# Kernel optimization log

Hardware: AMD Instinct MI355X
Metric: run time of the kernel (lower is better)

Reference implementation:

```python
import jax, jax.numpy as jnp
import numpy as np
import math

B, M, DM = 4, 4096, 1024
H, HD = 16, 64            # head_dim = hidden_dim // num_heads
SEG, DIL = 128, 2         # segment_size, dilation_rate
BLOCK_M = 64              # kernel query-block size (min(64, M))
SCALE = HD ** -0.5


def _hilbert_map(seq_len):
    # Faithful port of create_hilbert_mapping_fixed (boustrophedon scan).
    if seq_len <= 64:
        return np.arange(seq_len, dtype=np.int32)
    g = int(math.ceil(math.sqrt(seq_len)))
    mp = np.zeros(seq_len, dtype=np.int64)
    idx = 0
    for row in range(g):
        cols = range(g) if row % 2 == 0 else range(g - 1, -1, -1)
        for col in cols:
            if idx < seq_len:
                lp = row * g + col
                if lp < seq_len:
                    mp[lp] = idx
                    idx += 1
    for i in range(seq_len):
        if i >= idx:
            mp[i] = i
    return mp.astype(np.int32)


def setup_inputs() -> dict:
    key = jax.random.key(0)
    k1, k2, k3 = jax.random.split(key, 3)
    x = jax.random.normal(k1, (B, M, DM), jnp.float32)
    Wqkv = jax.random.normal(k2, (3 * DM, DM), jnp.float32) * 0.02
    Wout = jax.random.normal(k3, (DM, DM), jnp.float32) * 0.02
    hmap = jnp.asarray(_hilbert_map(M))
    return {"x": x, "Wqkv": Wqkv, "Wout": Wout, "hmap": hmap}


def _hilbert_attention(x, Wqkv, Wout, hmap):
    Bn, Mn, _ = x.shape
    qkv = x @ Wqkv.T                                   # [B,M,3*DM]
    qkv = qkv.reshape(Bn, Mn, 3, H, HD).transpose(2, 0, 3, 1, 4)
    q, k, v = qkv[0], qkv[1], qkv[2]                   # [B,H,M,HD]

    S = Mn // SEG           # number of segments
    T = SEG // DIL          # keys per segment (dilated offsets 0, DIL, 2*DIL, ...)
    NB = SEG // BLOCK_M     # query blocks per segment

    # Queries gathered through Hilbert map, pre-scaled (as in kernel).
    qh = q[:, :, hmap, :] * SCALE                      # [B,H,M,HD]

    # Dilated key positions per segment, gathered through Hilbert map.
    key_pos = (jnp.arange(S)[:, None] * SEG + jnp.arange(T)[None, :] * DIL).reshape(-1)
    kh = k[:, :, hmap[key_pos], :].reshape(Bn, H, S, T, HD)
    vh = v[:, :, hmap[key_pos], :].reshape(Bn, H, S, T, HD)

    # Scores per (query-block within segment, key): [B,H,S,NB,BLOCK_M,T]
    qs = qh.reshape(Bn, H, S, NB, BLOCK_M, HD)
    scores = jnp.einsum('bhsnqd,bhstd->bhsnqt', qs, kh)

    # Kernel quirk (faithful): per-KEY max taken over the 64-query block,
    # exp accumulated without rescaling -> NOT a true softmax.
    c = jnp.max(scores, axis=4, keepdims=True)         # max over query block
    w = jnp.exp(scores - c)
    num = jnp.einsum('bhsnqt,bhstd->bhsnqd', w, vh)
    den = 1e-10 + jnp.sum(w, axis=-1, keepdims=True)
    out = (num / den).reshape(Bn, H, Mn, HD)

    # Stored at linear (non-Hilbert) positions, then merged heads + out proj.
    out = out.transpose(0, 2, 1, 3).reshape(Bn, Mn, H * HD)
    return out @ Wout.T


def reference(x, Wqkv, Wout, hmap):
    return _hilbert_attention(x, Wqkv, Wout, hmap)
```

## Files before the change

kernel.cpp:

```cpp
#include <hip/hip_runtime.h>
#include <hip/hip_bf16.h>

#define BB 4
#define MM 4096
#define DM 1024
#define NH 16
#define HDIM 64
#define SEGSZ 128
#define NSEG 32
#define ROWS (BB*MM)
#define QKVC (3*DM)
#define KVROWS (BB*MM/2)
#define KVLD 2048
#define NX4  (ROWS*DM/4)
#define NW14 (QKVC*DM/4)
#define NW24 (DM*DM/4)

typedef __attribute__((ext_vector_type(8))) short bf16x8;
typedef __attribute__((ext_vector_type(4))) float f32x4;

__device__ inline unsigned short f2bf(float f) {
  __hip_bfloat16 h = __float2bfloat16(f);
  return *reinterpret_cast<unsigned short*>(&h);
}

__device__ __forceinline__ void gld16(const ushort* g, ushort* l) {
  __builtin_amdgcn_global_load_lds(
      (const __attribute__((address_space(1))) unsigned int*)g,
      (__attribute__((address_space(3))) unsigned int*)l,
      16, 0, 0);
}

__global__ __launch_bounds__(256) void cvt_all(const float4* __restrict__ x,
                                               const float4* __restrict__ w1,
                                               const float4* __restrict__ w2,
                                               ushort4* __restrict__ xo,
                                               ushort4* __restrict__ w1o,
                                               ushort4* __restrict__ w2o) {
  int i = blockIdx.x * 256 + threadIdx.x;
  const float4* src; ushort4* dst; int off;
  if (i < NX4)              { src = x;  dst = xo;  off = i; }
  else if (i < NX4 + NW14)  { src = w1; dst = w1o; off = i - NX4; }
  else                      { src = w2; dst = w2o; off = i - NX4 - NW14; }
  float4 v = src[off];
  ushort4 o;
  o.x = f2bf(v.x); o.y = f2bf(v.y); o.z = f2bf(v.z); o.w = f2bf(v.w);
  dst[off] = o;
}

__global__ __launch_bounds__(512) void gemm_qkv(const ushort* __restrict__ xbf,
                                                const ushort* __restrict__ wqkv,
                                                ushort* __restrict__ qhb,
                                                ushort* __restrict__ kvb,
                                                const int* __restrict__ hmap) {
  __shared__ __align__(16) ushort sAB[65536];
  __shared__ int sRow[256];

  const int blk = blockIdx.x;
  const int tid = threadIdx.x;
  const int lane = tid & 63;
  const int wave = tid >> 6;
  const int m16 = lane & 15;
  const int quad = lane >> 4;
  const int wm = wave >> 2;
  const int wn = wave & 3;

  const ushort* Bmat; ushort* C; int row0, col0, N;
  if (blk < 256) {
    row0 = (blk >> 2) * 256; col0 = (blk & 3) * 256;
    Bmat = wqkv; C = qhb; N = DM;
  } else {
    int j = blk - 256;
    row0 = (j >> 3) * 256; col0 = (j & 7) * 256;
    Bmat = wqkv + (size_t)DM * DM; C = kvb; N = KVLD;
  }

  if (tid < 256) {
    int m = row0 + tid, xrow;
    if (blk < 256) {
      int b = m >> 12, p = m & 4095;
      xrow = (b << 12) + hmap[p];
    } else {
      int b = m >> 11, idx = m & 2047;
      int ss = idx >> 6, tt = idx & 63;
      xrow = (b << 12) + hmap[ss * SEGSZ + 2 * tt];
    }
    sRow[tid] = xrow;
  }
  __syncthreads();

  const int f0 = wave * 64 + lane, f1 = 512 + f0;
  const int r0 = f0 >> 2, c0 = (f0 & 3) ^ ((f0 >> 3) & 3);
  const int r1 = f1 >> 2, c1 = (f1 & 3) ^ ((f1 >> 3) & 3);
  const ushort* pA0 = xbf + (size_t)sRow[r0] * DM + c0 * 8;
  const ushort* pA1 = xbf + (size_t)sRow[r1] * DM + c1 * 8;
  const ushort* pB0 = Bmat + (size_t)(col0 + r0) * DM + c0 * 8;
  const ushort* pB1 = Bmat + (size_t)(col0 + r1) * DM + c1 * 8;

  f32x4 acc[8][4] = {};

#define STAGE_A(T, KH, DB) do {                                              \
    gld16(pA0 + (T) * 64 + (KH) * 32,                                        \
          sAB + ((DB) * 2 + (KH)) * 8192 + wave * 512);                      \
    gld16(pA1 + (T) * 64 + (KH) * 32,                                        \
          sAB + ((DB) * 2 + (KH)) * 8192 + 4096 + wave * 512);               \
  } while (0)
#define STAGE_B(T, KH, DB) do {                                              \
    gld16(pB0 + (T) * 64 + (KH) * 32,                                        \
          sAB + 32768 + ((DB) * 2 + (KH)) * 8192 + wave * 512);              \
    gld16(pB1 + (T) * 64 + (KH) * 32,                                        \
          sAB + 32768 + ((DB) * 2 + (KH)) * 8192 + 4096 + wave * 512);       \
  } while (0)
#define VM6 asm volatile("s_waitcnt vmcnt(6)" ::: "memory")
#define VM8 asm volatile("s_waitcnt vmcnt(8)" ::: "memory")
#define VM0 asm volatile("s_waitcnt vmcnt(0)" ::: "memory")
#define NOPS ((void)0)

#define PH(TB, KH, CH, STAGE, VMA) do {                                      \
    const ushort* Ab = sAB + ((TB) * 2 + (KH)) * 8192;                       \
    const ushort* Bb = sAB + 32768 + ((TB) * 2 + (KH)) * 8192;               \
    bf16x8 af[8], bfv[2];                                                    \
    _Pragma("unroll")                                                        \
    for (int mf = 0; mf < 8; ++mf) {                                         \
      int r = wm * 128 + mf * 16 + m16;                                      \
      af[mf] = *(const bf16x8*)(Ab + r * 32 + ((quad ^ ((r >> 1) & 3)) << 3)); \
    }                                                                        \
    _Pragma("unroll")                                                        \
    for (int nf = 0; nf < 2; ++nf) {                                         \
      int r = wn * 64 + (CH) * 32 + nf * 16 + m16;                           \
      bfv[nf] = *(const bf16x8*)(Bb + r * 32 + ((quad ^ ((r >> 1) & 3)) << 3)); \
    }                                                                        \
    STAGE;                                                                   \
    VMA;                                                                     \
    __builtin_amdgcn_s_barrier();                                            \
    asm volatile("s_waitcnt lgkmcnt(0)" ::: "memory");                       \
    __builtin_amdgcn_sched_barrier(0);                                       \
    __builtin_amdgcn_s_setprio(1);                                           \
    _Pragma("unroll")                                                        \
    for (int mf = 0; mf < 8; ++mf)                                           \
      _Pragma("unroll")                                                      \
      for (int nf = 0; nf < 2; ++nf)                                         \
        acc[mf][(CH) * 2 + nf] = __builtin_amdgcn_mfma_f32_16x16x32_bf16(    \
            af[mf], bfv[nf], acc[mf][(CH) * 2 + nf], 0, 0, 0);               \
    __builtin_amdgcn_s_setprio(0);                                           \
    __builtin_amdgcn_s_barrier();                                            \
  } while (0)

  STAGE_A(0, 0, 0); STAGE_B(0, 0, 0);
  STAGE_A(0, 1, 0); STAGE_B(0, 1, 0);
  STAGE_A(1, 0, 1); STAGE_B(1, 0, 1);
  VM8;
  __builtin_amdgcn_s_barrier();

#pragma unroll 1
  for (int i = 0; i < 7; ++i) {
    const int t1 = 2 * i + 1, t2 = 2 * i + 2, t3 = 2 * i + 3;
    PH(0, 0, 0, STAGE_A(t1, 1, 1), NOPS);
    PH(0, 0, 1, STAGE_B(t1, 1, 1), VM6);
    PH(0, 1, 0, STAGE_A(t2, 0, 0), NOPS);
    PH(0, 1, 1, STAGE_B(t2, 0, 0), VM6);
    PH(1, 0, 0, STAGE_A(t2, 1, 0), NOPS);
    PH(1, 0, 1, STAGE_B(t2, 1, 0), VM6);
    PH(1, 1, 0, STAGE_A(t3, 0, 1), NOPS);
    PH(1, 1, 1, STAGE_B(t3, 0, 1), VM6);
  }
  PH(0, 0, 0, STAGE_A(15, 1, 1), NOPS);
  PH(0, 0, 1, STAGE_B(15, 1, 1), VM0);
  PH(0, 1, 0, NOPS, NOPS);
  PH(0, 1, 1, NOPS, NOPS);
  PH(1, 0, 0, NOPS, NOPS);
  PH(1, 0, 1, NOPS, NOPS);
  PH(1, 1, 0, NOPS, NOPS);
  PH(1, 1, 1, NOPS, NOPS);

#undef PH
#undef STAGE_A
#undef STAGE_B
#undef VM6
#undef VM8
#undef VM0
#undef NOPS

#pragma unroll
  for (int mf = 0; mf < 8; ++mf)
#pragma unroll
    for (int rr = 0; rr < 4; ++rr) {
      int row = row0 + wm * 128 + mf * 16 + quad * 4 + rr;
#pragma unroll
      for (int nf = 0; nf < 4; ++nf)
        C[(size_t)row * N + col0 + wn * 64 + nf * 16 + m16] = f2bf(acc[mf][nf][rr]);
    }
}

__global__ __launch_bounds__(256) void gemm_out(const ushort* __restrict__ A,
                                                const ushort* __restrict__ Bmat,
                                                float* __restrict__ C) {
  __shared__ __align__(16) ushort sA[128 * 32];
  __shared__ __align__(16) ushort sB[64 * 32];
  const int blk = blockIdx.x;
  const int row0 = (blk >> 4) * 128;
  const int col0 = (blk & 15) * 64;
  const int tid = threadIdx.x;
  const int lane = tid & 63;
  const int wave = tid >> 6;
  const int m16 = lane & 15;
  const int quad = lane >> 4;
  const int wr = (wave >> 1) * 64;
  const int wc = (wave & 1) * 32;

  f32x4 acc[4][2] = {};

  const int ch0 = wave * 64 + lane;
  const int ch1 = 256 + wave * 64 + lane;
  const int ra0 = ch0 >> 2, ka0 = (ch0 & 3) * 8;
  const int ra1 = ch1 >> 2, ka1 = (ch1 & 3) * 8;

  const ushort* pa0 = A + (size_t)(row0 + ra0) * DM + ka0;
  const ushort* pa1 = A + (size_t)(row0 + ra1) * DM + ka1;
  const ushort* pb0 = Bmat + (size_t)(col0 + ra0) * DM + ka0;
  ushort* lA0 = sA + wave * 512;
  ushort* lA1 = sA + 2048 + wave * 512;
  ushort* lB0 = sB + wave * 512;

  for (int kt = 0; kt < DM; kt += 32) {
    __syncthreads();
    gld16(pa0 + kt, lA0);
    gld16(pa1 + kt, lA1);
    gld16(pb0 + kt, lB0);
    __syncthreads();

    bf16x8 af[4], bfr[2];
#pragma unroll
    for (int i = 0; i < 4; ++i)
      af[i] = *(const bf16x8*)(sA + (wr + i * 16 + m16) * 32 + quad * 8);
#pragma unroll
    for (int j = 0; j < 2; ++j)
      bfr[j] = *(const bf16x8*)(sB + (wc + j * 16 + m16) * 32 + quad * 8);
#pragma unroll
    for (int i = 0; i < 4; ++i)
#pragma unroll
      for (int j = 0; j < 2; ++j)
        acc[i][j] = __builtin_amdgcn_mfma_f32_16x16x32_bf16(af[i], bfr[j], acc[i][j], 0, 0, 0);
  }

#pragma unroll
  for (int i = 0; i < 4; ++i)
#pragma unroll
    for (int r = 0; r < 4; ++r) {
      int row = row0 + wr + i * 16 + quad * 4 + r;
#pragma unroll
      for (int j = 0; j < 2; ++j)
        C[(size_t)row * DM + col0 + wc + j * 16 + m16] = acc[i][j][r];
    }
}

__global__ __launch_bounds__(256) void attn_kernel(const ushort* __restrict__ qh,
                                                   const ushort* __restrict__ kv,
                                                   ushort* __restrict__ out) {
  __shared__ __align__(16) ushort sQW[128 * 72];
  __shared__ __align__(16) ushort sK[64 * 72];
  __shared__ __align__(16) ushort sVT[64 * 72];
  __shared__ float sCmaxW[4 * 64];
  __shared__ float sDen[128];

  const int bid = blockIdx.x;
  const int s  = bid & 31;
  const int h  = (bid >> 5) & 15;
  const int b  = bid >> 9;
  const int tid = threadIdx.x;
  const int lane = tid & 63;
  const int wave = tid >> 6;
  const int m16 = lane & 15;
  const int quad = lane >> 4;
  const int qb = wave * 32;
  const int hb = wave >> 1;

  {
    const int qr = tid >> 1;
    const int qc = (tid & 1) * 32;
    const ushort* qrow = qh + (size_t)(b * MM + s * SEGSZ + qr) * DM + h * HDIM + qc;
    *(uint4*)(sQW + qr * 72 + qc)      = ((const uint4*)qrow)[0];
    *(uint4*)(sQW + qr * 72 + qc + 8)  = ((const uint4*)qrow)[1];
    *(uint4*)(sQW + qr * 72 + qc + 16) = ((const uint4*)qrow)[2];
    *(uint4*)(sQW + qr * 72 + qc + 24) = ((const uint4*)qrow)[3];

    const int r = tid >> 2;
    const int c = (tid & 3) * 16;
    const ushort* krow = kv + (size_t)(b * (MM/2) + s * 64 + r) * KVLD + h * HDIM + c;
    const ushort* vrow = krow + DM;
    *(uint4*)(sK + r * 72 + c)     = ((const uint4*)krow)[0];
    *(uint4*)(sK + r * 72 + c + 8) = ((const uint4*)krow)[1];
    ushort vv[16];
    *(uint4*)(vv)     = ((const uint4*)vrow)[0];
    *(uint4*)(vv + 8) = ((const uint4*)vrow)[1];
#pragma unroll
    for (int u = 0; u < 16; ++u) sVT[(c + u) * 72 + r] = vv[u];
  }
  __syncthreads();

  f32x4 sc[2][4];
  {
    bf16x8 aq[2][2], bk[4][2];
#pragma unroll
    for (int ks = 0; ks < 2; ++ks) {
#pragma unroll
      for (int ib = 0; ib < 2; ++ib)
        aq[ib][ks] = *(const bf16x8*)(sQW + (qb + ib * 16 + m16) * 72 + ks * 32 + quad * 8);
#pragma unroll
      for (int j = 0; j < 4; ++j)
        bk[j][ks] = *(const bf16x8*)(sK + (j * 16 + m16) * 72 + ks * 32 + quad * 8);
    }
#pragma unroll
    for (int ib = 0; ib < 2; ++ib)
#pragma unroll
      for (int j = 0; j < 4; ++j) {
        f32x4 a = {};
        a = __builtin_amdgcn_mfma_f32_16x16x32_bf16(aq[ib][0], bk[j][0], a, 0, 0, 0);
        a = __builtin_amdgcn_mfma_f32_16x16x32_bf16(aq[ib][1], bk[j][1], a, 0, 0, 0);
        sc[ib][j] = a * 0.125f;
      }
  }

#pragma unroll
  for (int j = 0; j < 4; ++j) {
    float m = -1e30f;
#pragma unroll
    for (int ib = 0; ib < 2; ++ib)
#pragma unroll
      for (int r = 0; r < 4; ++r) m = fmaxf(m, sc[ib][j][r]);
    m = fmaxf(m, __shfl_xor(m, 16));
    m = fmaxf(m, __shfl_xor(m, 32));
    if (quad == 0) sCmaxW[wave * 64 + j * 16 + m16] = m;
  }
  __syncthreads();

  {
    float part[2][4] = {};
#pragma unroll
    for (int j = 0; j < 4; ++j) {
      const int col = j * 16 + m16;
      float c0 = fmaxf(sCmaxW[hb * 128 + col], sCmaxW[hb * 128 + 64 + col]);
#pragma unroll
      for (int ib = 0; ib < 2; ++ib)
#pragma unroll
        for (int r = 0; r < 4; ++r) {
          float ww = __expf(sc[ib][j][r] - c0);
          sc[ib][j][r] = ww;
          part[ib][r] += ww;
        }
    }
#pragma unroll
    for (int ib = 0; ib < 2; ++ib)
#pragma unroll
      for (int r = 0; r < 4; ++r) {
        float p = part[ib][r];
        p += __shfl_xor(p, 1); p += __shfl_xor(p, 2);
        p += __shfl_xor(p, 4); p += __shfl_xor(p, 8);
        if (m16 == 0) sDen[qb + ib * 16 + quad * 4 + r] = p;
      }
#pragma unroll
    for (int ib = 0; ib < 2; ++ib)
#pragma unroll
      for (int j = 0; j < 4; ++j)
#pragma unroll
        for (int r = 0; r < 4; ++r)
          sQW[(qb + ib * 16 + quad * 4 + r) * 72 + j * 16 + m16] = f2bf(sc[ib][j][r]);
  }
  __syncthreads();

  f32x4 o[2][4] = {};
  {
    bf16x8 aw[2][2], bv[4][2];
#pragma unroll
    for (int ks = 0; ks < 2; ++ks) {
#pragma unroll
      for (int ib = 0; ib < 2; ++ib)
        aw[ib][ks] = *(const bf16x8*)(sQW + (qb + ib * 16 + m16) * 72 + ks * 32 + quad * 8);
#pragma unroll
      for (int j = 0; j < 4; ++j)
        bv[j][ks] = *(const bf16x8*)(sVT + (j * 16 + m16) * 72 + ks * 32 + quad * 8);
    }
#pragma unroll
    for (int ib = 0; ib < 2; ++ib)
#pragma unroll
      for (int j = 0; j < 4; ++j) {
        o[ib][j] = __builtin_amdgcn_mfma_f32_16x16x32_bf16(aw[ib][0], bv[j][0], o[ib][j], 0, 0, 0);
        o[ib][j] = __builtin_amdgcn_mfma_f32_16x16x32_bf16(aw[ib][1], bv[j][1], o[ib][j], 0, 0, 0);
      }
  }

#pragma unroll
  for (int ib = 0; ib < 2; ++ib)
#pragma unroll
    for (int r = 0; r < 4; ++r) {
      const int lrow = qb + ib * 16 + quad * 4 + r;
      float rd = 1.0f / (1e-10f + sDen[lrow]);
      ushort* op = out + (size_t)(b * MM + s * SEGSZ + lrow) * DM + h * HDIM + m16;
#pragma unroll
      for (int j = 0; j < 4; ++j)
        op[j * 16] = f2bf(o[ib][j][r] * rd);
    }
}

extern "C" void kernel_launch(void* const* d_in, const int* in_sizes, int n_in,
                              void* d_out, int out_size, void* d_ws, size_t ws_size,
                              hipStream_t stream) {
  const float* x    = (const float*)d_in[0];
  const float* wqkv = (const float*)d_in[1];
  const float* wout = (const float*)d_in[2];
  const int*   hmap = (const int*)d_in[3];
  float* outp = (float*)d_out;

  ushort* xbf    = (ushort*)d_ws;
  ushort* wqkvbf = xbf + (size_t)ROWS * DM;
  ushort* woutbf = wqkvbf + (size_t)QKVC * DM;
  ushort* qhb    = woutbf + (size_t)DM * DM;
  ushort* kvb    = qhb + (size_t)ROWS * DM;
  ushort* attn   = kvb + (size_t)KVROWS * KVLD;

  cvt_all<<<(NX4 + NW14 + NW24 + 255) / 256, 256, 0, stream>>>(
      (const float4*)x, (const float4*)wqkv, (const float4*)wout,
      (ushort4*)xbf, (ushort4*)wqkvbf, (ushort4*)woutbf);

  gemm_qkv<<<512, 512, 0, stream>>>(xbf, wqkvbf, qhb, kvb, hmap);

  attn_kernel<<<BB * NH * NSEG, 256, 0, stream>>>(qhb, kvb, attn);

  gemm_out<<<2048, 256, 0, stream>>>(attn, woutbf, outp);
}
```

Baseline: 293.2 us.

## Software-pipeline LDS fragment reads one phase ahead in QKV GEMM

Restructures the QKV GEMM main loop so that A and B fragments for the next phase are read from shared memory into double-buffered registers (af0/af1, bv0/bv1) while the current phase's MFMAs run. The lgkmcnt wait is relaxed so MFMAs only wait on the older fragment loads, and the vmcnt thresholds are adjusted to match. The swizzle offset is hoisted into a single precomputed value. This aims to hide LDS latency behind matrix math, at the cost of more VGPRs and tricky barrier and waitcnt ordering that could cause hazards or spills.

Result: no change. 298.2 us (+1.7%).

```diff
diff --git a/kernel.cpp b/kernel.cpp
--- a/kernel.cpp
+++ b/kernel.cpp
@@ -97,43 +97,42 @@
   const ushort* pB0 = Bmat + (size_t)(col0 + r0) * DM + c0 * 8;
   const ushort* pB1 = Bmat + (size_t)(col0 + r1) * DM + c1 * 8;
 
+  const int sw = ((quad ^ ((m16 >> 1) & 3)) << 3);
+
   f32x4 acc[8][4] = {};
+  bf16x8 af0[8], af1[8], bv0[2], bv1[2];
+
+#define AB_(DB, KH) (sAB + ((DB) * 2 + (KH)) * 8192)
+#define BB_(DB, KH) (sAB + 32768 + ((DB) * 2 + (KH)) * 8192)
+#define RD(BASE, ROW) (*(const bf16x8*)((BASE) + (ROW) * 32 + sw))
 
 #define STAGE_A(T, KH, DB) do {                                              \
-    gld16(pA0 + (T) * 64 + (KH) * 32,                                        \
-          sAB + ((DB) * 2 + (KH)) * 8192 + wave * 512);                      \
-    gld16(pA1 + (T) * 64 + (KH) * 32,                                        \
-          sAB + ((DB) * 2 + (KH)) * 8192 + 4096 + wave * 512);               \
+    gld16(pA0 + (T) * 64 + (KH) * 32, AB_(DB, KH) + wave * 512);             \
+    gld16(pA1 + (T) * 64 + (KH) * 32, AB_(DB, KH) + 4096 + wave * 512);      \
   } while (0)
 #define STAGE_B(T, KH, DB) do {                                              \
-    gld16(pB0 + (T) * 64 + (KH) * 32,                                        \
-          sAB + 32768 + ((DB) * 2 + (KH)) * 8192 + wave * 512);              \
-    gld16(pB1 + (T) * 64 + (KH) * 32,                                        \
-          sAB + 32768 + ((DB) * 2 + (KH)) * 8192 + 4096 + wave * 512);       \
+    gld16(pB0 + (T) * 64 + (KH) * 32, BB_(DB, KH) + wave * 512);             \
+    gld16(pB1 + (T) * 64 + (KH) * 32, BB_(DB, KH) + 4096 + wave * 512);      \
   } while (0)
-#define VM6 asm volatile("s_waitcnt vmcnt(6)" ::: "memory")
+#define VM4 asm volatile("s_waitcnt vmcnt(4)" ::: "memory")
 #define VM8 asm volatile("s_waitcnt vmcnt(8)" ::: "memory")
 #define VM0 asm volatile("s_waitcnt vmcnt(0)" ::: "memory")
 #define NOPS ((void)0)
 
-#define PH(TB, KH, CH, STAGE, VMA) do {                                      \
-    const ushort* Ab = sAB + ((TB) * 2 + (KH)) * 8192;                       \
-    const ushort* Bb = sAB + 32768 + ((TB) * 2 + (KH)) * 8192;               \
-    bf16x8 af[8], bfv[2];                                                    \
-    _Pragma("unroll")                                                        \
-    for (int mf = 0; mf < 8; ++mf) {                                         \
-      int r = wm * 128 + mf * 16 + m16;                                      \
-      af[mf] = *(const bf16x8*)(Ab + r * 32 + ((quad ^ ((r >> 1) & 3)) << 3)); \
+#define PHX(AFU, BVU, CH, DO_B, BVF, BbN, NCH, DO_A, AFF, AFH, AbN, STAGE, VMA, LGK) do { \
+    if (DO_B) {                                                              \
+      _Pragma("unroll")                                                      \
+      for (int nf = 0; nf < 2; ++nf)                                         \
+        BVF[nf] = RD((BbN), wn * 64 + (NCH) * 32 + nf * 16 + m16);           \
     }                                                                        \
-    _Pragma("unroll")                                                        \
-    for (int nf = 0; nf < 2; ++nf) {                                         \
-      int r = wn * 64 + (CH) * 32 + nf * 16 + m16;                           \
-      bfv[nf] = *(const bf16x8*)(Bb + r * 32 + ((quad ^ ((r >> 1) & 3)) << 3)); \
+    if (DO_A) {                                                              \
+      _Pragma("unroll")                                                      \
+      for (int mf = 0; mf < 4; ++mf)                                         \
+        AFF[(AFH) * 4 + mf] = RD((AbN), wm * 128 + ((AFH) * 4 + mf) * 16 + m16); \
     }                                                                        \
-    STAGE;                                                                   \
-    VMA;                                                                     \
+    STAGE; VMA;                                                              \
     __builtin_amdgcn_s_barrier();                                            \
-    asm volatile("s_waitcnt lgkmcnt(0)" ::: "memory");                       \
+    asm volatile("s_waitcnt lgkmcnt(" #LGK ")" ::: "memory");                \
     __builtin_amdgcn_sched_barrier(0);                                       \
     __builtin_amdgcn_s_setprio(1);                                           \
     _Pragma("unroll")                                                        \
@@ -141,7 +140,7 @@
       _Pragma("unroll")                                                      \
       for (int nf = 0; nf < 2; ++nf)                                         \
         acc[mf][(CH) * 2 + nf] = __builtin_amdgcn_mfma_f32_16x16x32_bf16(    \
-            af[mf], bfv[nf], acc[mf][(CH) * 2 + nf], 0, 0, 0);               \
+            AFU[mf], BVU[nf], acc[mf][(CH) * 2 + nf], 0, 0, 0);              \
     __builtin_amdgcn_s_setprio(0);                                           \
     __builtin_amdgcn_s_barrier();                                            \
   } while (0)
@@ -151,35 +150,42 @@
   STAGE_A(1, 0, 1); STAGE_B(1, 0, 1);
   VM8;
   __builtin_amdgcn_s_barrier();
+#pragma unroll
+  for (int mf = 0; mf < 8; ++mf) af0[mf] = RD(AB_(0, 0), wm * 128 + mf * 16 + m16);
+#pragma unroll
+  for (int nf = 0; nf < 2; ++nf) bv0[nf] = RD(BB_(0, 0), wn * 64 + nf * 16 + m16);
 
 #pragma unroll 1
   for (int i = 0; i < 7; ++i) {
     const int t1 = 2 * i + 1, t2 = 2 * i + 2, t3 = 2 * i + 3;
-    PH(0, 0, 0, STAGE_A(t1, 1, 1), NOPS);
-    PH(0, 0, 1, STAGE_B(t1, 1, 1), VM6);
-    PH(0, 1, 0, STAGE_A(t2, 0, 0), NOPS);
-    PH(0, 1, 1, STAGE_B(t2, 0, 0), VM6);
-    PH(1, 0, 0, STAGE_A(t2, 1, 0), NOPS);
-    PH(1, 0, 1, STAGE_B(t2, 1, 0), VM6);
-    PH(1, 1, 0, STAGE_A(t3, 0, 1), NOPS);
-    PH(1, 1, 1, STAGE_B(t3, 0, 1), VM6);
-  }
-  PH(0, 0, 0, STAGE_A(15, 1, 1), NOPS);
-  PH(0, 0, 1, STAGE_B(15, 1, 1), VM0);
-  PH(0, 1, 0, NOPS, NOPS);
-  PH(0, 1, 1, NOPS, NOPS);
-  PH(1, 0, 0, NOPS, NOPS);
-  PH(1, 0, 1, NOPS, NOPS);
-  PH(1, 1, 0, NOPS, NOPS);
-  PH(1, 1, 1, NOPS, NOPS);
-
-#undef PH
+    PHX(af0, bv0, 0, 1, bv1, BB_(0,0), 1, 1, af1, 0, AB_(0,1), STAGE_A(t1,1,1), NOPS, 6);
+    PHX(af0, bv1, 1, 1, bv0, BB_(0,1), 0, 1, af1, 1, AB_(0,1), STAGE_B(t1,1,1), VM4,  6);
+    PHX(af1, bv0, 0, 1, bv1, BB_(0,1), 1, 1, af0, 0, AB_(1,0), STAGE_A(t2,0,0), NOPS, 6);
+    PHX(af1, bv1, 1, 1, bv0, BB_(1,0), 0, 1, af0, 1, AB_(1,0), STAGE_B(t2,0,0), VM4,  6);
+    PHX(af0, bv0, 0, 1, bv1, BB_(1,0), 1, 1, af1, 0, AB_(1,1), STAGE_A(t2,1,0), NOPS, 6);
+    PHX(af0, bv1, 1, 1, bv0, BB_(1,1), 0, 1, af1, 1, AB_(1,1), STAGE_B(t2,1,0), VM4,  6);
+    PHX(af1, bv0, 0, 1, bv1, BB_(1,1), 1, 1, af0, 0, AB_(0,0), STAGE_A(t3,0,1), NOPS, 6);
+    PHX(af1, bv1, 1, 1, bv0, BB_(0,0), 0, 1, af0, 1, AB_(0,0), STAGE_B(t3,0,1), VM4,  6);
+  }
+  PHX(af0, bv0, 0, 1, bv1, BB_(0,0), 1, 1, af1, 0, AB_(0,1), STAGE_A(15,1,1), NOPS, 6);
+  PHX(af0, bv1, 1, 1, bv0, BB_(0,1), 0, 1, af1, 1, AB_(0,1), STAGE_B(15,1,1), VM0,  6);
+  PHX(af1, bv0, 0, 1, bv1, BB_(0,1), 1, 1, af0, 0, AB_(1,0), NOPS, NOPS, 6);
+  PHX(af1, bv1, 1, 1, bv0, BB_(1,0), 0, 1, af0, 1, AB_(1,0), NOPS, NOPS, 6);
+  PHX(af0, bv0, 0, 1, bv1, BB_(1,0), 1, 1, af1, 0, AB_(1,1), NOPS, NOPS, 6);
+  PHX(af0, bv1, 1, 1, bv0, BB_(1,1), 0, 1, af1, 1, AB_(1,1), NOPS, NOPS, 6);
+  PHX(af1, bv0, 0, 1, bv1, BB_(1,1), 1, 0, af0, 0, AB_(0,0), NOPS, NOPS, 2);
+  PHX(af1, bv1, 1, 0, bv0, BB_(0,0), 0, 0, af0, 1, AB_(0,0), NOPS, NOPS, 0);
+
+#undef PHX
 #undef STAGE_A
 #undef STAGE_B
-#undef VM6
+#undef VM4
 #undef VM8
 #undef VM0
 #undef NOPS
+#undef RD
+#undef AB_
+#undef BB_
 
 #pragma unroll
   for (int mf = 0; mf < 8; ++mf)
```
